# Performance work log

Hardware: AMD Instinct MI355X
Metric: run time of the kernel (lower is better)

Reference implementation:

```python
import jax, jax.numpy as jnp
import numpy as np

TEMPERATURE = 0.02  # args.temperature


def setup_inputs() -> dict:
    key = jax.random.key(0)
    bs, seq_len, n_vars = 64, 512, 8
    k_positive, k_negative = 3, 16
    B = bs * n_vars            # 512
    P, D = 64, 128             # patch_num, d_model
    k1, k2, k3 = jax.random.split(key, 3)
    similarity_matrix = jax.random.normal(k1, (B, k_positive + k_negative), dtype=jnp.float32)
    # rows [0:B] are the original batch embeddings, rows [B:] are the positives
    p_enc_out = jax.random.normal(k2, (B * (1 + k_positive), P, D), dtype=jnp.float32)
    negative_index = jax.random.randint(k3, (B, k_negative), 0, B)
    return {
        "similarity_matrix": similarity_matrix,
        "p_enc_out": p_enc_out,
        "negative_index": negative_index,
        "bs": bs,
        "seq_len": seq_len,
        "n_vars": n_vars,
        "k_positive": k_positive,
        "k_negative": k_negative,
    }


def reference(similarity_matrix, p_enc_out, negative_index, bs, seq_len, n_vars, k_positive, k_negative):
    B = bs * n_vars
    P = p_enc_out.shape[-2]
    # temperature-scaled softmax over (positives ++ negatives) similarity scores
    w = jax.nn.softmax(similarity_matrix / TEMPERATURE, axis=-1)  # [B, kp+kn]
    # positives: rows B: of p_enc_out, flattened per sample -> [B, kp, P*D]
    pos = p_enc_out[B:].reshape(B, k_positive, -1)
    # negatives: gather rows of the original batch by index -> [B, kn, P*D]
    neg = p_enc_out[:B][negative_index].reshape(B, k_negative, -1)
    # weighted aggregation: two batched matvecs, summed
    rebuild = (jnp.einsum('bk,bkd->bd', w[:, :k_positive], pos)
               + jnp.einsum('bk,bkd->bd', w[:, k_positive:], neg))  # [B, P*D]
    return rebuild.reshape(B, P, -1)
```

## Files before the change

### kernel.cpp

```cpp
#include <hip/hip_runtime.h>
#include <hip/hip_bf16.h>
#include <math.h>

#define BATCH   512
#define KP      3
#define KN      16
#define KTOT    (KP + KN)
#define PD      8192
#define INV_T   50.0f

#define SPLIT   8
#define CHUNK   (PD / SPLIT)
#define THREADS 256

__global__ __launch_bounds__(THREADS)
void agg_rebuild_kernel(const float* __restrict__ sim,
                        const float* __restrict__ p_enc,
                        const int*   __restrict__ neg_idx,
                        float*       __restrict__ out) {
    const int b    = blockIdx.x / SPLIT;
    const int part = blockIdx.x % SPLIT;
    const int tid  = threadIdx.x;

    __shared__ float        s_w[KTOT];
    __shared__ const float* s_row[KTOT];

    if (tid == 0) {
        float v[KTOT];
        float m = -INFINITY;
        #pragma unroll
        for (int k = 0; k < KTOT; ++k) {
            v[k] = sim[(size_t)b * KTOT + k] * INV_T;
            m = fmaxf(m, v[k]);
        }
        float s = 0.0f;
        #pragma unroll
        for (int k = 0; k < KTOT; ++k) {
            v[k] = __expf(v[k] - m);
            s += v[k];
        }
        const float inv = 1.0f / s;
        #pragma unroll
        for (int k = 0; k < KTOT; ++k) s_w[k] = v[k] * inv;
    }

    if (tid < KTOT) {
        int row;
        if (tid < KP) row = BATCH + b * KP + tid;
        else          row = neg_idx[(size_t)b * KN + (tid - KP)];
        s_row[tid] = p_enc + (size_t)row * PD;
    }
    __syncthreads();

    const int d = part * CHUNK + tid * 4;
    float4 acc = make_float4(0.f, 0.f, 0.f, 0.f);
    #pragma unroll
    for (int k = 0; k < KTOT; ++k) {
        const float  w = s_w[k];
        const float4 x = *reinterpret_cast<const float4*>(s_row[k] + d);
        acc.x = fmaf(w, x.x, acc.x);
        acc.y = fmaf(w, x.y, acc.y);
        acc.z = fmaf(w, x.z, acc.z);
        acc.w = fmaf(w, x.w, acc.w);
    }
    *reinterpret_cast<float4*>(out + (size_t)b * PD + d) = acc;
}

extern "C" void kernel_launch(void* const* d_in, const int* in_sizes, int n_in,
                              void* d_out, int out_size, void* d_ws, size_t ws_size,
                              hipStream_t stream) {
    const float* sim     = (const float*)d_in[0];
    const float* p_enc   = (const float*)d_in[1];
    const int*   neg_idx = (const int*)d_in[2];
    float*       out     = (float*)d_out;

    dim3 grid(BATCH * SPLIT);
    dim3 block(THREADS);
    agg_rebuild_kernel<<<grid, block, 0, stream>>>(sim, p_enc, neg_idx, out);
}
```

Before: 21.12 us.

## Compute softmax per thread, halve split, use 8-wide nontemporal loads and stores

```diff
diff --git a/kernel.cpp b/kernel.cpp
--- a/kernel.cpp
+++ b/kernel.cpp
@@ -9,61 +9,70 @@
 #define PD      8192
 #define INV_T   50.0f
 
-#define SPLIT   8
+#define SPLIT   4
 #define CHUNK   (PD / SPLIT)
 #define THREADS 256
+
+typedef float f32x4 __attribute__((ext_vector_type(4)));
 
 __global__ __launch_bounds__(THREADS)
 void agg_rebuild_kernel(const float* __restrict__ sim,
                         const float* __restrict__ p_enc,
                         const int*   __restrict__ neg_idx,
                         float*       __restrict__ out) {
-    const int b    = blockIdx.x / SPLIT;
-    const int part = blockIdx.x % SPLIT;
+    const int b    = blockIdx.x >> 2;
+    const int part = blockIdx.x & (SPLIT-1);
     const int tid  = threadIdx.x;
 
-    __shared__ float        s_w[KTOT];
-    __shared__ const float* s_row[KTOT];
+    float w[KTOT];
+    float m = -INFINITY;
+    #pragma unroll
+    for (int k = 0; k < KTOT; ++k) {
+        w[k] = sim[b * KTOT + k] * INV_T;
+        m = fmaxf(m, w[k]);
+    }
+    float s = 0.0f;
+    #pragma unroll
+    for (int k = 0; k < KTOT; ++k) {
+        w[k] = __expf(w[k] - m);
+        s += w[k];
+    }
+    const float inv = 1.0f / s;
 
-    if (tid == 0) {
-        float v[KTOT];
-        float m = -INFINITY;
-        #pragma unroll
-        for (int k = 0; k < KTOT; ++k) {
-            v[k] = sim[(size_t)b * KTOT + k] * INV_T;
-            m = fmaxf(m, v[k]);
-        }
-        float s = 0.0f;
-        #pragma unroll
-        for (int k = 0; k < KTOT; ++k) {
-            v[k] = __expf(v[k] - m);
-            s += v[k];
-        }
-        const float inv = 1.0f / s;
-        #pragma unroll
-        for (int k = 0; k < KTOT; ++k) s_w[k] = v[k] * inv;
+    const float* rowp[KTOT];
+    #pragma unroll
+    for (int k = 0; k < KP; ++k)
+        rowp[k] = p_enc + (size_t)(BATCH + b * KP + k) * PD;
+    #pragma unroll
+    for (int k = 0; k < KN; ++k)
+        rowp[KP + k] = p_enc + (size_t)neg_idx[b * KN + k] * PD;
+
+    const int d = part * CHUNK + tid * 8;
+    f32x4 acc0 = {0.f, 0.f, 0.f, 0.f};
+    f32x4 acc1 = {0.f, 0.f, 0.f, 0.f};
+
+    #pragma unroll
+    for (int k = 0; k < KP; ++k) {
+        const float wk = w[k] * inv;
+        const f32x4* p = reinterpret_cast<const f32x4*>(rowp[k] + d);
+        const f32x4 x0 = __builtin_nontemporal_load(p);
+        const f32x4 x1 = __builtin_nontemporal_load(p + 1);
+        acc0 += wk * x0;
+        acc1 += wk * x1;
+    }
+    #pragma unroll
+    for (int k = KP; k < KTOT; ++k) {
+        const float wk = w[k] * inv;
+        const f32x4* p = reinterpret_cast<const f32x4*>(rowp[k] + d);
+        const f32x4 x0 = p[0];
+        const f32x4 x1 = p[1];
+        acc0 += wk * x0;
+        acc1 += wk * x1;
     }
 
-    if (tid < KTOT) {
-        int row;
-        if (tid < KP) row = BATCH + b * KP + tid;
-        else          row = neg_idx[(size_t)b * KN + (tid - KP)];
-        s_row[tid] = p_enc + (size_t)row * PD;
-    }
-    __syncthreads();
-
-    const int d = part * CHUNK + tid * 4;
-    float4 acc = make_float4(0.f, 0.f, 0.f, 0.f);
-    #pragma unroll
-    for (int k = 0; k < KTOT; ++k) {
-        const float  w = s_w[k];
-        const float4 x = *reinterpret_cast<const float4*>(s_row[k] + d);
-        acc.x = fmaf(w, x.x, acc.x);
-        acc.y = fmaf(w, x.y, acc.y);
-        acc.z = fmaf(w, x.z, acc.z);
-        acc.w = fmaf(w, x.w, acc.w);
-    }
-    *reinterpret_cast<float4*>(out + (size_t)b * PD + d) = acc;
+    f32x4* o = reinterpret_cast<f32x4*>(out + (size_t)b * PD + d);
+    __builtin_nontemporal_store(acc0, o);
+    __builtin_nontemporal_store(acc1, o + 1);
 }
 
 extern "C" void kernel_launch(void* const* d_in, const int* in_sizes, int n_in,
```

Result: slower. 30.81 us (+45.9%).
